# Kernel tuning notes

Hardware: AMD Instinct MI355X
Metric: run time of the kernel (lower is better)

The kernel has to match this reference:

```python
import jax, jax.numpy as jnp
import numpy as np

EMBED_DIM = 1024
NUM_HEADS = 16
HEAD_DIM = EMBED_DIM // NUM_HEADS


def setup_inputs() -> dict:
    key = jax.random.key(0)
    k1, k2, k3, k4 = jax.random.split(key, 4)
    B, T, C = 4, 2048, EMBED_DIM
    scale = 1.0 / np.sqrt(C)
    x = jax.random.normal(k1, (B, T, C), dtype=jnp.float32)
    # nn.Linear(C, 3C, bias=False): weight [3C, C]
    w_qkv = jax.random.normal(k2, (3 * C, C), dtype=jnp.float32) * scale
    # nn.Linear(C, C) with bias
    w_out = jax.random.normal(k3, (C, C), dtype=jnp.float32) * scale
    b_out = jax.random.normal(k4, (C,), dtype=jnp.float32) * 0.01
    return {"x": x, "w_qkv": w_qkv, "w_out": w_out, "b_out": b_out}


def reference(x, w_qkv, w_out, b_out):
    B, T, C = x.shape
    H, D = NUM_HEADS, HEAD_DIM
    qkv = x @ w_qkv.T                      # [B,T,3C]
    q, k, v = jnp.split(qkv, 3, axis=-1)
    # [B,T,C] -> [B,H,T,D]
    q = q.reshape(B, T, H, D).transpose(0, 2, 1, 3)
    k = k.reshape(B, T, H, D).transpose(0, 2, 1, 3)
    v = v.reshape(B, T, H, D).transpose(0, 2, 1, 3)
    scores = jnp.einsum("bhqd,bhkd->bhqk", q, k) / jnp.sqrt(jnp.float32(D))
    causal = jnp.tril(jnp.ones((T, T), dtype=bool))
    scores = jnp.where(causal, scores, -jnp.inf)
    attn = jax.nn.softmax(scores, axis=-1)  # dropout is identity in eval mode
    out = jnp.einsum("bhqk,bhkd->bhqd", attn, v)
    out = out.transpose(0, 2, 1, 3).reshape(B, T, C)
    return out @ w_out.T + b_out
```

## Files before the change

kernel.cpp:

```cpp
#include <hip/hip_runtime.h>
#include <hip/hip_bf16.h>

typedef __bf16 bf16_t;
typedef __bf16 bf16x4 __attribute__((ext_vector_type(4)));
typedef __bf16 bf16x8 __attribute__((ext_vector_type(8)));
typedef float f32x4 __attribute__((ext_vector_type(4)));

#define MFMA16(a, b, c) __builtin_amdgcn_mfma_f32_16x16x32_bf16(a, b, c, 0, 0, 0)

__device__ __forceinline__ void gld16(const bf16_t* g, bf16_t* l) {
  __builtin_amdgcn_global_load_lds(
      (const __attribute__((address_space(1))) unsigned int*)(const void*)g,
      (__attribute__((address_space(3))) unsigned int*)(void*)l, 16, 0, 0);
}

__global__ __launch_bounds__(256) void cvt3_f32_bf16(
    const float* __restrict__ s0, bf16_t* __restrict__ d0, long long n0,
    const float* __restrict__ s1, bf16_t* __restrict__ d1, long long n1,
    const float* __restrict__ s2, bf16_t* __restrict__ d2, long long n2) {
  const long long t0 = ((long long)blockIdx.x * 256 + threadIdx.x) * 8;
  const long long stride = (long long)gridDim.x * 256 * 8;
#pragma unroll 1
  for (int seg = 0; seg < 3; ++seg) {
    const float* s = (seg == 0) ? s0 : (seg == 1) ? s1 : s2;
    bf16_t* d = (seg == 0) ? d0 : (seg == 1) ? d1 : d2;
    const long long n = (seg == 0) ? n0 : (seg == 1) ? n1 : n2;
    if (!d) continue;
    for (long long i = t0; i < n; i += stride) {
      f32x4 a = *(const f32x4*)(s + i);
      f32x4 b = *(const f32x4*)(s + i + 4);
      bf16x8 r;
#pragma unroll
      for (int e = 0; e < 4; ++e) {
        r[e] = (bf16_t)a[e];
        r[4 + e] = (bf16_t)b[e];
      }
      *(bf16x8*)(d + i) = r;
    }
  }
}

template <bool WF32, typename TC, bool BIAS>
__global__ __launch_bounds__(256, 3) void gemm_async(
    const bf16_t* __restrict__ A, int lda, const void* __restrict__ Wv,
    const float* __restrict__ bias, TC* __restrict__ C, int ldc,
    int M, int N, int K) {
  __shared__ bf16_t As[128 * 64];
  __shared__ bf16_t Bs[128 * 64];

  const int tid = threadIdx.x;
  const int i = tid & 63;
  const int w = tid >> 6;
  const int l16 = tid & 15;
  const int quad = (tid >> 4) & 3;
  const int wm = w & 1;
  const int wn = w >> 1;

  const int nwg = gridDim.x * gridDim.y;
  int wg = blockIdx.y * gridDim.x + blockIdx.x;
  if ((nwg & 7) == 0) wg = (wg & 7) * (nwg >> 3) + (wg >> 3);
  const int m0 = (wg / gridDim.x) * 128;
  const int n0 = (wg % gridDim.x) * 128;

  const int srw = i >> 3;
  const int ssl = ((i & 7) ^ srw) << 3;
  const bf16_t* ag = A + (size_t)(m0 + w * 32 + srw) * lda + ssl;

  const bf16_t* bg = nullptr;
  const float* wfg = nullptr;
  int bsrow = 0, bchunk = 0;
  if (!WF32) {
    bg = (const bf16_t*)Wv + (size_t)(n0 + w * 32 + srw) * K + ssl;
  } else {
    bsrow = tid >> 1;
    bchunk = tid & 1;
    wfg = (const float*)Wv + (size_t)(n0 + bsrow) * K + bchunk * 32;
  }

  f32x4 acc[4][4] = {};

  for (int kt = 0; kt < (K >> 6); ++kt) {
    if (kt) __syncthreads();
#pragma unroll
    for (int g = 0; g < 4; ++g)
      gld16(ag + (size_t)(g * 8) * lda + kt * 64, &As[(w * 32 + g * 8) * 64]);
    if (!WF32) {
#pragma unroll
      for (int g = 0; g < 4; ++g)
        gld16(bg + (size_t)(g * 8) * K + kt * 64, &Bs[(w * 32 + g * 8) * 64]);
    } else {
#pragma unroll
      for (int j = 0; j < 4; ++j) {
        f32x4 a = *(const f32x4*)(wfg + kt * 64 + j * 8);
        f32x4 b = *(const f32x4*)(wfg + kt * 64 + j * 8 + 4);
        bf16x8 r;
#pragma unroll
        for (int e = 0; e < 4; ++e) {
          r[e] = (bf16_t)a[e];
          r[4 + e] = (bf16_t)b[e];
        }
        const int slot = (bchunk * 4 + j) ^ (bsrow & 7);
        *(bf16x8*)&Bs[bsrow * 64 + slot * 8] = r;
      }
    }
    __syncthreads();

#pragma unroll
    for (int ks = 0; ks < 2; ++ks) {
      bf16x8 af[4], bfr[4];
#pragma unroll
      for (int t = 0; t < 4; ++t) {
        const int ar = wm * 64 + t * 16 + l16;
        const int br = wn * 64 + t * 16 + l16;
        const int slot = ((ks * 4 + quad) ^ (l16 & 7)) * 8;
        af[t] = *(const bf16x8*)&As[ar * 64 + slot];
        bfr[t] = *(const bf16x8*)&Bs[br * 64 + slot];
      }
      __builtin_amdgcn_s_setprio(1);
#pragma unroll
      for (int mi = 0; mi < 4; ++mi)
#pragma unroll
        for (int ni = 0; ni < 4; ++ni)
          acc[mi][ni] = MFMA16(af[mi], bfr[ni], acc[mi][ni]);
      __builtin_amdgcn_s_setprio(0);
    }
  }

#pragma unroll
  for (int ni = 0; ni < 4; ++ni) {
    const int col = n0 + wn * 64 + ni * 16 + l16;
    const float bv = BIAS ? bias[col] : 0.0f;
#pragma unroll
    for (int mi = 0; mi < 4; ++mi) {
      const int row = m0 + wm * 64 + mi * 16 + quad * 4;
#pragma unroll
      for (int r = 0; r < 4; ++r)
        C[(size_t)(row + r) * ldc + col] = (TC)(acc[mi][ni][r] + bv);
    }
  }
}

__global__ __launch_bounds__(512, 4) void attn_mfma(bf16_t* __restrict__ qkv) {
  constexpr int T = 2048, C3 = 3072, C = 1024;
  __shared__ bf16_t Ks[128 * 72];
  __shared__ bf16_t Vt[64 * 136];
  __shared__ bf16_t Ps[8 * 16 * 136];

  const int tid = threadIdx.x;
  const int wave = tid >> 6;
  const int lane = tid & 63;
  const int l16 = tid & 15;
  const int quad = (tid >> 4) & 3;
  const int p = blockIdx.x;
  const int b = blockIdx.y >> 4;
  const int h = blockIdx.y & 15;
  bf16_t* base = qkv + (size_t)b * T * C3;

  const float QSCALE = 0.125f * 1.44269504088896340736f;

  const int krow = wave * 32 + (lane >> 1);
  const int kcol = (lane & 1) * 32;
  const int wv = wave - 4;
  const int vtok = ((wv & 2) << 5) + lane;
  const int vd0 = (wv & 1) * 32;

  bf16_t* pw = &Ps[wave * 16 * 136];

  bf16x8 st0, st1, st2, st3;

  for (int s = 0; s < 2; ++s) {
    const int qt = (s == 0) ? p : 15 - p;
    const int Q0 = qt * 128;
    const int qlo = Q0 + wave * 16;

    bf16x8 qf[2];
    {
      const bf16_t* qp = base + (size_t)(qlo + l16) * C3 + h * 64 + quad * 8;
      bf16x8 a = *(const bf16x8*)qp;
      bf16x8 c = *(const bf16x8*)(qp + 32);
#pragma unroll
      for (int e = 0; e < 8; ++e) {
        a[e] = (bf16_t)((float)a[e] * QSCALE);
        c[e] = (bf16_t)((float)c[e] * QSCALE);
      }
      qf[0] = a;
      qf[1] = c;
    }

    f32x4 Of[4] = {};
    float mrow = -1e30f;
    float lrow = 0.f;

    if (wave < 4) {
      const bf16_t* kp = base + (size_t)krow * C3 + C + h * 64 + kcol;
      st0 = *(const bf16x8*)kp;
      st1 = *(const bf16x8*)(kp + 8);
      st2 = *(const bf16x8*)(kp + 16);
      st3 = *(const bf16x8*)(kp + 24);
    } else {
      const bf16_t* vp = base + (size_t)vtok * C3 + 2 * C + h * 64 + vd0;
      st0 = *(const bf16x8*)vp;
      st1 = *(const bf16x8*)(vp + 8);
      st2 = *(const bf16x8*)(vp + 16);
      st3 = *(const bf16x8*)(vp + 24);
    }

    for (int j0 = 0; j0 <= Q0; j0 += 128) {
      __syncthreads();
      if (wave < 4) {
        *(bf16x8*)&Ks[krow * 72 + kcol] = st0;
        *(bf16x8*)&Ks[krow * 72 + kcol + 8] = st1;
        *(bf16x8*)&Ks[krow * 72 + kcol + 16] = st2;
        *(bf16x8*)&Ks[krow * 72 + kcol + 24] = st3;
      } else {
#pragma unroll
        for (int e = 0; e < 8; ++e) {
          Vt[(vd0 + e) * 136 + vtok] = st0[e];
          Vt[(vd0 + 8 + e) * 136 + vtok] = st1[e];
          Vt[(vd0 + 16 + e) * 136 + vtok] = st2[e];
          Vt[(vd0 + 24 + e) * 136 + vtok] = st3[e];
        }
      }
      if (j0 + 128 <= Q0) {
        const int jn = j0 + 128;
        if (wave < 4) {
          const bf16_t* kp =
              base + (size_t)(jn + krow) * C3 + C + h * 64 + kcol;
          st0 = *(const bf16x8*)kp;
          st1 = *(const bf16x8*)(kp + 8);
          st2 = *(const bf16x8*)(kp + 16);
          st3 = *(const bf16x8*)(kp + 24);
        } else {
          const bf16_t* vp =
              base + (size_t)(jn + vtok) * C3 + 2 * C + h * 64 + vd0;
          st0 = *(const bf16x8*)vp;
          st1 = *(const bf16x8*)(vp + 8);
          st2 = *(const bf16x8*)(vp + 16);
          st3 = *(const bf16x8*)(vp + 24);
        }
      }
      __syncthreads();

      float Sv[8][4];
      int ntlim = 8;
      if (j0 + 128 <= qlo) {
        __builtin_amdgcn_s_setprio(1);
#pragma unroll
        for (int nt = 0; nt < 8; ++nt) {
          f32x4 sacc = {};
#pragma unroll
          for (int s2 = 0; s2 < 2; ++s2) {
            bf16x8 kf = *(const bf16x8*)&Ks[(nt * 16 + l16) * 72 + s2 * 32 +
                                            quad * 8];
            sacc = MFMA16(kf, qf[s2], sacc);
          }
#pragma unroll
          for (int r = 0; r < 4; ++r) Sv[nt][r] = sacc[r];
        }
        __builtin_amdgcn_s_setprio(0);
      } else {
        ntlim = ((qlo + 15 - j0) >> 4) + 1;
        const int qrow = qlo + l16;
        __builtin_amdgcn_s_setprio(1);
#pragma unroll
        for (int nt = 0; nt < 8; ++nt) {
          if (nt < ntlim) {
            f32x4 sacc = {};
#pragma unroll
            for (int s2 = 0; s2 < 2; ++s2) {
              bf16x8 kf = *(const bf16x8*)&Ks[(nt * 16 + l16) * 72 + s2 * 32 +
                                              quad * 8];
              sacc = MFMA16(kf, qf[s2], sacc);
            }
            const int keyb = j0 + nt * 16 + quad * 4;
#pragma unroll
            for (int r = 0; r < 4; ++r)
              Sv[nt][r] = (keyb + r > qrow) ? -1e30f : sacc[r];
          } else {
#pragma unroll
            for (int r = 0; r < 4; ++r) Sv[nt][r] = -1e30f;
          }
        }
        __builtin_amdgcn_s_setprio(0);
      }

      float v = -1e30f;
#pragma unroll
      for (int nt = 0; nt < 8; ++nt)
        v = fmaxf(v, fmaxf(fmaxf(Sv[nt][0], Sv[nt][1]),
                           fmaxf(Sv[nt][2], Sv[nt][3])));
      v = fmaxf(v, __shfl_xor(v, 16));
      v = fmaxf(v, __shfl_xor(v, 32));

      if (__any(v > mrow)) {
        const float mnew = fmaxf(mrow, v);
        const float alpha = __builtin_amdgcn_exp2f(mrow - mnew);
        mrow = mnew;
        lrow *= alpha;
        float ar[4];
#pragma unroll
        for (int r = 0; r < 4; ++r) ar[r] = __shfl(alpha, quad * 4 + r, 16);
#pragma unroll
        for (int dt = 0; dt < 4; ++dt)
#pragma unroll
          for (int r = 0; r < 4; ++r) Of[dt][r] *= ar[r];
      }

      float rs = 0.f;
#pragma unroll
      for (int nt = 0; nt < 8; ++nt) {
        bf16x4 pk;
        float r0 = __builtin_amdgcn_exp2f(Sv[nt][0] - mrow);
        float r1 = __builtin_amdgcn_exp2f(Sv[nt][1] - mrow);
        float r2 = __builtin_amdgcn_exp2f(Sv[nt][2] - mrow);
        float r3 = __builtin_amdgcn_exp2f(Sv[nt][3] - mrow);
        pk[0] = (bf16_t)r0;
        pk[1] = (bf16_t)r1;
        pk[2] = (bf16_t)r2;
        pk[3] = (bf16_t)r3;
        rs += (r0 + r1) + (r2 + r3);
        *(bf16x4*)&pw[l16 * 136 + nt * 16 + quad * 4] = pk;
      }
      rs += __shfl_xor(rs, 16);
      rs += __shfl_xor(rs, 32);
      lrow += rs;

      const int kslim = (ntlim + 1) >> 1;
      bf16x8 pf[4];
#pragma unroll
      for (int ks = 0; ks < 4; ++ks)
        pf[ks] = *(const bf16x8*)&pw[l16 * 136 + ks * 32 + quad * 8];
      __builtin_amdgcn_s_setprio(1);
#pragma unroll
      for (int ks = 0; ks < 4; ++ks) {
        if (ks < kslim) {
#pragma unroll
          for (int dt = 0; dt < 4; ++dt) {
            bf16x8 vf = *(const bf16x8*)&Vt[(dt * 16 + l16) * 136 + ks * 32 +
                                            quad * 8];
            Of[dt] = MFMA16(pf[ks], vf, Of[dt]);
          }
        }
      }
      __builtin_amdgcn_s_setprio(0);
    }

    float lr[4];
#pragma unroll
    for (int r = 0; r < 4; ++r) lr[r] = __shfl(lrow, quad * 4 + r, 16);
    const int t = Q0 + wave * 16 + quad * 4;
#pragma unroll
    for (int r = 0; r < 4; ++r) {
      const float inv = 1.0f / lr[r];
      bf16_t* op = base + (size_t)(t + r) * C3 + h * 64 + l16;
#pragma unroll
      for (int dt = 0; dt < 4; ++dt)
        op[dt * 16] = (bf16_t)(Of[dt][r] * inv);
    }
  }
}

extern "C" void kernel_launch(void* const* d_in, const int* in_sizes, int n_in,
                              void* d_out, int out_size, void* d_ws,
                              size_t ws_size, hipStream_t stream) {
  constexpr int B = 4, T = 2048, C = 1024;
  constexpr int M = B * T;

  const float* x = (const float*)d_in[0];
  const float* w_qkv = (const float*)d_in[1];
  const float* w_out = (const float*)d_in[2];
  const float* b_out = (const float*)d_in[3];
  for (int i = 0; i < n_in; ++i) {
    const long long s = in_sizes[i];
    if (s == (long long)M * C) x = (const float*)d_in[i];
    else if (s == (long long)3 * C * C) w_qkv = (const float*)d_in[i];
    else if (s == (long long)C * C) w_out = (const float*)d_in[i];
    else if (s == C) b_out = (const float*)d_in[i];
  }

  bf16_t* xb = (bf16_t*)d_out;
  bf16_t* wqb = xb + (size_t)M * C;
  bf16_t* qkv = (bf16_t*)d_ws;
  bf16_t* wob = qkv + (size_t)M * 3 * C;
  const bool ws_ok =
      ws_size >= (size_t)M * 3 * C * 2 + (size_t)C * C * 2;

  cvt3_f32_bf16<<<1024, 256, 0, stream>>>(
      x, xb, (long long)M * C, w_qkv, wqb, 3LL * C * C, w_out,
      ws_ok ? wob : nullptr, (long long)C * C);

  gemm_async<false, bf16_t, false>
      <<<dim3(3 * C / 128, M / 128), 256, 0, stream>>>(
          xb, C, wqb, nullptr, qkv, 3 * C, M, 3 * C, C);

  attn_mfma<<<dim3(8, B * 16), 512, 0, stream>>>(qkv);

  if (ws_ok)
    gemm_async<false, float, true><<<dim3(C / 128, M / 128), 256, 0, stream>>>(
        qkv, 3 * C, wob, b_out, (float*)d_out, C, M, C, C);
  else
    gemm_async<true, float, true><<<dim3(C / 128, M / 128), 256, 0, stream>>>(
        qkv, 3 * C, w_out, b_out, (float*)d_out, C, M, C, C);
}
```

Measured before the change: 243.7 us.

## Rewrite attention with 32x32 MFMA tiles, register-resident P, swizzled LDS

Measured after the change: 245.7 us. Within noise of the previous version (+0.8%).

```diff
diff --git a/kernel.cpp b/kernel.cpp
--- a/kernel.cpp
+++ b/kernel.cpp
@@ -5,14 +5,18 @@
 typedef __bf16 bf16x4 __attribute__((ext_vector_type(4)));
 typedef __bf16 bf16x8 __attribute__((ext_vector_type(8)));
 typedef float f32x4 __attribute__((ext_vector_type(4)));
+typedef float f32x16 __attribute__((ext_vector_type(16)));
 
 #define MFMA16(a, b, c) __builtin_amdgcn_mfma_f32_16x16x32_bf16(a, b, c, 0, 0, 0)
+#define MFMA32(a, b, c) __builtin_amdgcn_mfma_f32_32x32x16_bf16(a, b, c, 0, 0, 0)
 
 __device__ __forceinline__ void gld16(const bf16_t* g, bf16_t* l) {
   __builtin_amdgcn_global_load_lds(
       (const __attribute__((address_space(1))) unsigned int*)(const void*)g,
       (__attribute__((address_space(3))) unsigned int*)(void*)l, 16, 0, 0);
 }
+
+__device__ __forceinline__ int swz8(int row) { return ((row >> 3) & 3) << 3; }
 
 __global__ __launch_bounds__(256) void cvt3_f32_bf16(
     const float* __restrict__ s0, bf16_t* __restrict__ d0, long long n0,
@@ -140,17 +144,16 @@
   }
 }
 
-__global__ __launch_bounds__(512, 4) void attn_mfma(bf16_t* __restrict__ qkv) {
+__global__ __launch_bounds__(256, 2) void attn_mfma(bf16_t* __restrict__ qkv) {
   constexpr int T = 2048, C3 = 3072, C = 1024;
-  __shared__ bf16_t Ks[128 * 72];
-  __shared__ bf16_t Vt[64 * 136];
-  __shared__ bf16_t Ps[8 * 16 * 136];
+  __shared__ bf16_t Ks[64 * 72];
+  __shared__ bf16_t Vt[64 * 72];
 
   const int tid = threadIdx.x;
   const int wave = tid >> 6;
   const int lane = tid & 63;
-  const int l16 = tid & 15;
-  const int quad = (tid >> 4) & 3;
+  const int l31 = lane & 31;
+  const int hi = lane >> 5;
   const int p = blockIdx.x;
   const int b = blockIdx.y >> 4;
   const int h = blockIdx.y & 15;
@@ -158,41 +161,36 @@
 
   const float QSCALE = 0.125f * 1.44269504088896340736f;
 
-  const int krow = wave * 32 + (lane >> 1);
-  const int kcol = (lane & 1) * 32;
-  const int wv = wave - 4;
-  const int vtok = ((wv & 2) << 5) + lane;
-  const int vd0 = (wv & 1) * 32;
-
-  bf16_t* pw = &Ps[wave * 16 * 136];
+  const int ktok = tid >> 1;
+  const int kd0 = (tid & 1) * 32;
+  const int vtok = lane;
+  const int vd0 = (wave - 2) * 32;
 
   bf16x8 st0, st1, st2, st3;
 
   for (int s = 0; s < 2; ++s) {
     const int qt = (s == 0) ? p : 15 - p;
     const int Q0 = qt * 128;
-    const int qlo = Q0 + wave * 16;
-
-    bf16x8 qf[2];
+    const int qlo = Q0 + wave * 32;
+    const int jmax = Q0 + 64;
+
+    bf16x8 qf[4];
     {
-      const bf16_t* qp = base + (size_t)(qlo + l16) * C3 + h * 64 + quad * 8;
-      bf16x8 a = *(const bf16x8*)qp;
-      bf16x8 c = *(const bf16x8*)(qp + 32);
-#pragma unroll
-      for (int e = 0; e < 8; ++e) {
-        a[e] = (bf16_t)((float)a[e] * QSCALE);
-        c[e] = (bf16_t)((float)c[e] * QSCALE);
-      }
-      qf[0] = a;
-      qf[1] = c;
-    }
-
-    f32x4 Of[4] = {};
-    float mrow = -1e30f;
-    float lrow = 0.f;
-
-    if (wave < 4) {
-      const bf16_t* kp = base + (size_t)krow * C3 + C + h * 64 + kcol;
+      const bf16_t* qp = base + (size_t)(qlo + l31) * C3 + h * 64 + hi * 8;
+#pragma unroll
+      for (int kd = 0; kd < 4; ++kd) {
+        bf16x8 a = *(const bf16x8*)(qp + kd * 16);
+#pragma unroll
+        for (int e = 0; e < 8; ++e) a[e] = (bf16_t)((float)a[e] * QSCALE);
+        qf[kd] = a;
+      }
+    }
+
+    f32x16 Of0 = {}, Of1 = {};
+    float mrow = -1e30f, lrow = 0.f;
+
+    if (wave < 2) {
+      const bf16_t* kp = base + (size_t)ktok * C3 + C + h * 64 + kd0;
       st0 = *(const bf16x8*)kp;
       st1 = *(const bf16x8*)(kp + 8);
       st2 = *(const bf16x8*)(kp + 16);
@@ -205,27 +203,28 @@
       st3 = *(const bf16x8*)(vp + 24);
     }
 
-    for (int j0 = 0; j0 <= Q0; j0 += 128) {
+    for (int j0 = 0; j0 <= jmax; j0 += 64) {
       __syncthreads();
-      if (wave < 4) {
-        *(bf16x8*)&Ks[krow * 72 + kcol] = st0;
-        *(bf16x8*)&Ks[krow * 72 + kcol + 8] = st1;
-        *(bf16x8*)&Ks[krow * 72 + kcol + 16] = st2;
-        *(bf16x8*)&Ks[krow * 72 + kcol + 24] = st3;
+      if (wave < 2) {
+        *(bf16x8*)&Ks[ktok * 72 + ((kd0 + 0) ^ swz8(ktok))] = st0;
+        *(bf16x8*)&Ks[ktok * 72 + ((kd0 + 8) ^ swz8(ktok))] = st1;
+        *(bf16x8*)&Ks[ktok * 72 + ((kd0 + 16) ^ swz8(ktok))] = st2;
+        *(bf16x8*)&Ks[ktok * 72 + ((kd0 + 24) ^ swz8(ktok))] = st3;
       } else {
 #pragma unroll
         for (int e = 0; e < 8; ++e) {
-          Vt[(vd0 + e) * 136 + vtok] = st0[e];
-          Vt[(vd0 + 8 + e) * 136 + vtok] = st1[e];
-          Vt[(vd0 + 16 + e) * 136 + vtok] = st2[e];
-          Vt[(vd0 + 24 + e) * 136 + vtok] = st3[e];
-        }
-      }
-      if (j0 + 128 <= Q0) {
-        const int jn = j0 + 128;
-        if (wave < 4) {
-          const bf16_t* kp =
-              base + (size_t)(jn + krow) * C3 + C + h * 64 + kcol;
+          int d0 = vd0 + e, d1 = vd0 + 8 + e, d2 = vd0 + 16 + e,
+              d3 = vd0 + 24 + e;
+          Vt[d0 * 72 + (vtok ^ swz8(d0))] = st0[e];
+          Vt[d1 * 72 + (vtok ^ swz8(d1))] = st1[e];
+          Vt[d2 * 72 + (vtok ^ swz8(d2))] = st2[e];
+          Vt[d3 * 72 + (vtok ^ swz8(d3))] = st3[e];
+        }
+      }
+      if (j0 + 64 <= jmax) {
+        const int jn = j0 + 64;
+        if (wave < 2) {
+          const bf16_t* kp = base + (size_t)(jn + ktok) * C3 + C + h * 64 + kd0;
           st0 = *(const bf16x8*)kp;
           st1 = *(const bf16x8*)(kp + 8);
           st2 = *(const bf16x8*)(kp + 16);
@@ -241,55 +240,38 @@
       }
       __syncthreads();
 
-      float Sv[8][4];
-      int ntlim = 8;
-      if (j0 + 128 <= qlo) {
-        __builtin_amdgcn_s_setprio(1);
-#pragma unroll
-        for (int nt = 0; nt < 8; ++nt) {
-          f32x4 sacc = {};
-#pragma unroll
-          for (int s2 = 0; s2 < 2; ++s2) {
-            bf16x8 kf = *(const bf16x8*)&Ks[(nt * 16 + l16) * 72 + s2 * 32 +
-                                            quad * 8];
-            sacc = MFMA16(kf, qf[s2], sacc);
+      if (qlo + 31 < j0) continue;
+
+      f32x16 Sa0 = {}, Sa1 = {};
+      __builtin_amdgcn_s_setprio(1);
+#pragma unroll
+      for (int kd = 0; kd < 4; ++kd) {
+        const int c = (kd * 16 + hi * 8);
+        bf16x8 k0 = *(const bf16x8*)&Ks[l31 * 72 + (c ^ swz8(l31))];
+        bf16x8 k1 = *(const bf16x8*)&Ks[(32 + l31) * 72 + (c ^ swz8(32 + l31))];
+        Sa0 = MFMA32(k0, qf[kd], Sa0);
+        Sa1 = MFMA32(k1, qf[kd], Sa1);
+      }
+      __builtin_amdgcn_s_setprio(0);
+
+      if (j0 + 63 > qlo) {
+        const int qrow = qlo + l31;
+#pragma unroll
+        for (int g = 0; g < 4; ++g)
+#pragma unroll
+          for (int j = 0; j < 4; ++j) {
+            const int key0 = j0 + 8 * g + 4 * hi + j;
+            if (key0 > qrow) Sa0[4 * g + j] = -1e30f;
+            if (key0 + 32 > qrow) Sa1[4 * g + j] = -1e30f;
           }
-#pragma unroll
-          for (int r = 0; r < 4; ++r) Sv[nt][r] = sacc[r];
-        }
-        __builtin_amdgcn_s_setprio(0);
-      } else {
-        ntlim = ((qlo + 15 - j0) >> 4) + 1;
-        const int qrow = qlo + l16;
-        __builtin_amdgcn_s_setprio(1);
-#pragma unroll
-        for (int nt = 0; nt < 8; ++nt) {
-          if (nt < ntlim) {
-            f32x4 sacc = {};
-#pragma unroll
-            for (int s2 = 0; s2 < 2; ++s2) {
-              bf16x8 kf = *(const bf16x8*)&Ks[(nt * 16 + l16) * 72 + s2 * 32 +
-                                              quad * 8];
-              sacc = MFMA16(kf, qf[s2], sacc);
-            }
-            const int keyb = j0 + nt * 16 + quad * 4;
-#pragma unroll
-            for (int r = 0; r < 4; ++r)
-              Sv[nt][r] = (keyb + r > qrow) ? -1e30f : sacc[r];
-          } else {
-#pragma unroll
-            for (int r = 0; r < 4; ++r) Sv[nt][r] = -1e30f;
-          }
-        }
-        __builtin_amdgcn_s_setprio(0);
       }
 
       float v = -1e30f;
 #pragma unroll
-      for (int nt = 0; nt < 8; ++nt)
-        v = fmaxf(v, fmaxf(fmaxf(Sv[nt][0], Sv[nt][1]),
-                           fmaxf(Sv[nt][2], Sv[nt][3])));
-      v = fmaxf(v, __shfl_xor(v, 16));
+      for (int r2 = 0; r2 < 16; ++r2) {
+        v = fmaxf(v, Sa0[r2]);
+        v = fmaxf(v, Sa1[r2]);
+      }
       v = fmaxf(v, __shfl_xor(v, 32));
 
       if (__any(v > mrow)) {
@@ -297,65 +279,91 @@
         const float alpha = __builtin_amdgcn_exp2f(mrow - mnew);
         mrow = mnew;
         lrow *= alpha;
-        float ar[4];
-#pragma unroll
-        for (int r = 0; r < 4; ++r) ar[r] = __shfl(alpha, quad * 4 + r, 16);
-#pragma unroll
-        for (int dt = 0; dt < 4; ++dt)
-#pragma unroll
-          for (int r = 0; r < 4; ++r) Of[dt][r] *= ar[r];
+#pragma unroll
+        for (int r2 = 0; r2 < 16; ++r2) {
+          Of0[r2] *= alpha;
+          Of1[r2] *= alpha;
+        }
       }
 
       float rs = 0.f;
-#pragma unroll
-      for (int nt = 0; nt < 8; ++nt) {
-        bf16x4 pk;
-        float r0 = __builtin_amdgcn_exp2f(Sv[nt][0] - mrow);
-        float r1 = __builtin_amdgcn_exp2f(Sv[nt][1] - mrow);
-        float r2 = __builtin_amdgcn_exp2f(Sv[nt][2] - mrow);
-        float r3 = __builtin_amdgcn_exp2f(Sv[nt][3] - mrow);
-        pk[0] = (bf16_t)r0;
-        pk[1] = (bf16_t)r1;
-        pk[2] = (bf16_t)r2;
-        pk[3] = (bf16_t)r3;
-        rs += (r0 + r1) + (r2 + r3);
-        *(bf16x4*)&pw[l16 * 136 + nt * 16 + quad * 4] = pk;
-      }
-      rs += __shfl_xor(rs, 16);
+      bf16x4 pk0[4], pk1[4];
+#pragma unroll
+      for (int g = 0; g < 4; ++g) {
+        bf16x4 a4, b4;
+#pragma unroll
+        for (int j = 0; j < 4; ++j) {
+          float p0 = __builtin_amdgcn_exp2f(Sa0[4 * g + j] - mrow);
+          float p1 = __builtin_amdgcn_exp2f(Sa1[4 * g + j] - mrow);
+          rs += p0 + p1;
+          a4[j] = (bf16_t)p0;
+          b4[j] = (bf16_t)p1;
+        }
+        pk0[g] = a4;
+        pk1[g] = b4;
+      }
       rs += __shfl_xor(rs, 32);
       lrow += rs;
 
-      const int kslim = (ntlim + 1) >> 1;
-      bf16x8 pf[4];
-#pragma unroll
-      for (int ks = 0; ks < 4; ++ks)
-        pf[ks] = *(const bf16x8*)&pw[l16 * 136 + ks * 32 + quad * 8];
+      union U {
+        bf16x4 v;
+        long long ll;
+      };
+      bf16x8 pfr[4];
+#pragma unroll
+      for (int kb = 0; kb < 2; ++kb) {
+        const bf16x4 q0 = kb ? pk1[0] : pk0[0];
+        const bf16x4 q1 = kb ? pk1[1] : pk0[1];
+        const bf16x4 q2 = kb ? pk1[2] : pk0[2];
+        const bf16x4 q3 = kb ? pk1[3] : pk0[3];
+        U ua;
+        ua.v = hi ? q0 : q1;
+        U ra;
+        ra.ll = __shfl_xor(ua.ll, 32);
+        U ub;
+        ub.v = hi ? q2 : q3;
+        U rb;
+        rb.ll = __shfl_xor(ub.ll, 32);
+        const bf16x4 lo0 = hi ? ra.v : q0;
+        const bf16x4 hi0v = hi ? q1 : ra.v;
+        const bf16x4 lo1 = hi ? rb.v : q2;
+        const bf16x4 hi1v = hi ? q3 : rb.v;
+        bf16x8 f0, f1;
+#pragma unroll
+        for (int j = 0; j < 4; ++j) {
+          f0[j] = lo0[j];
+          f0[4 + j] = hi0v[j];
+          f1[j] = lo1[j];
+          f1[4 + j] = hi1v[j];
+        }
+        pfr[kb * 2 + 0] = f0;
+        pfr[kb * 2 + 1] = f1;
+      }
+
       __builtin_amdgcn_s_setprio(1);
 #pragma unroll
-      for (int ks = 0; ks < 4; ++ks) {
-        if (ks < kslim) {
-#pragma unroll
-          for (int dt = 0; dt < 4; ++dt) {
-            bf16x8 vf = *(const bf16x8*)&Vt[(dt * 16 + l16) * 136 + ks * 32 +
-                                            quad * 8];
-            Of[dt] = MFMA16(pf[ks], vf, Of[dt]);
-          }
-        }
+      for (int kdt = 0; kdt < 4; ++kdt) {
+        const int c = (kdt * 16 + hi * 8);
+        bf16x8 v0 = *(const bf16x8*)&Vt[l31 * 72 + (c ^ swz8(l31))];
+        bf16x8 v1 = *(const bf16x8*)&Vt[(32 + l31) * 72 + (c ^ swz8(32 + l31))];
+        Of0 = MFMA32(v0, pfr[kdt], Of0);
+        Of1 = MFMA32(v1, pfr[kdt], Of1);
       }
       __builtin_amdgcn_s_setprio(0);
     }
 
-    float lr[4];
-#pragma unroll
-    for (int r = 0; r < 4; ++r) lr[r] = __shfl(lrow, quad * 4 + r, 16);
-    const int t = Q0 + wave * 16 + quad * 4;
-#pragma unroll
-    for (int r = 0; r < 4; ++r) {
-      const float inv = 1.0f / lr[r];
-      bf16_t* op = base + (size_t)(t + r) * C3 + h * 64 + l16;
-#pragma unroll
-      for (int dt = 0; dt < 4; ++dt)
-        op[dt * 16] = (bf16_t)(Of[dt][r] * inv);
+    const float inv = 1.0f / lrow;
+    bf16_t* op = base + (size_t)(qlo + l31) * C3 + h * 64;
+#pragma unroll
+    for (int g = 0; g < 4; ++g) {
+      bf16x4 o0, o1;
+#pragma unroll
+      for (int j = 0; j < 4; ++j) {
+        o0[j] = (bf16_t)(Of0[4 * g + j] * inv);
+        o1[j] = (bf16_t)(Of1[4 * g + j] * inv);
+      }
+      *(bf16x4*)&op[8 * g + 4 * hi] = o0;
+      *(bf16x4*)&op[32 + 8 * g + 4 * hi] = o1;
     }
   }
 }
@@ -393,7 +401,7 @@
       <<<dim3(3 * C / 128, M / 128), 256, 0, stream>>>(
           xb, C, wqb, nullptr, qkv, 3 * C, M, 3 * C, C);
 
-  attn_mfma<<<dim3(8, B * 16), 512, 0, stream>>>(qkv);
+  attn_mfma<<<dim3(8, B * 16), 256, 0, stream>>>(qkv);
 
   if (ws_ok)
     gemm_async<false, float, true><<<dim3(C / 128, M / 128), 256, 0, stream>>>(
```
